# Kernel tuning notes

Measured on AMD Instinct MI355X. Metric: run time of the kernel, lower is better.

The kernel has to match this reference:

```python
import jax, jax.numpy as jnp
import numpy as np

H = 12          # trees_num / n_heads
D_WEIGHT = 0.1  # opt['d_weight']
NEG = -1e9


def setup_inputs() -> dict:
    key = jax.random.key(0)
    ks = jax.random.split(key, 6)
    B, N, D = 8, 512, 768
    inp = {}
    inp["input"] = jax.random.normal(ks[0], (B, N, D), dtype=jnp.float32)
    inp["src_mask"] = jax.random.randint(ks[1], (B, 1, N), 0, 2).astype(jnp.int32)
    inp["dep_emb"] = jax.random.normal(ks[2], (B, N, N), dtype=jnp.float32)
    s = 1.0 / np.sqrt(D)
    inp["Wq"] = jax.random.normal(ks[3], (D, D), dtype=jnp.float32) * s
    inp["bq"] = jnp.zeros((D,), dtype=jnp.float32)
    inp["Wk"] = jax.random.normal(ks[4], (D, D), dtype=jnp.float32) * s
    inp["bk"] = jnp.zeros((D,), dtype=jnp.float32)
    return inp


def reference(input, src_mask, dep_emb, Wq, bq, Wk, bk):
    B, N, D = input.shape
    dk = D // H
    # Q/K projections -> [B, H, N, dk]
    q = (input @ Wq + bq).reshape(B, N, H, dk).transpose(0, 2, 1, 3)
    k = (input @ Wk + bk).reshape(B, N, H, dk).transpose(0, 2, 1, 3)
    # scaled scores [B, H, N, N]
    scores = jnp.einsum("bhqd,bhkd->bhqk", q, k) / jnp.sqrt(jnp.asarray(dk, input.dtype))
    # blend with dependency bias: dep_emb [B,N,N] -> [B,1,N,N]
    scores = (1.0 - D_WEIGHT) * scores + D_WEIGHT * dep_emb[:, None, :, :]
    # mask: src_mask [B,1,N] -> [B,1,1,N]; masked_fill(mask==0, -1e9)
    scores = jnp.where(src_mask[:, None, :, :] == 0, NEG, scores)
    p_attn = jax.nn.softmax(scores, axis=-1)  # [B, H, N, N]
    # original returns list of per-head [B,N,N]; full tensor is equivalent
    return p_attn
```

## Files before the change

### kernel.cpp

```cpp
#include <hip/hip_runtime.h>


typedef _Float16 f16;
typedef _Float16 f16x4 __attribute__((ext_vector_type(4)));
typedef _Float16 f16x8 __attribute__((ext_vector_type(8)));
typedef float    f32x4 __attribute__((ext_vector_type(4)));

#define NTOK   512
#define DMODEL 768
#define BATCH  8
#define NHEAD  12
#define NEGV   (-1e9f)
#define DEPS   516

#define GLOAD_LDS16(g, l)                                                        \
    __builtin_amdgcn_global_load_lds(                                            \
        (const __attribute__((address_space(1))) void*)(g),                      \
        (__attribute__((address_space(3))) void*)(l), 16, 0, 0)

__global__ __launch_bounds__(256)
void prep_kernel(const float* __restrict__ X, f16* __restrict__ Xh,
                 const float* __restrict__ Wq, const float* __restrict__ Wk,
                 f16* __restrict__ Wt) {
    const int bx = blockIdx.x;
    if (bx < 3072) {
        const size_t i = ((size_t)bx * 256 + threadIdx.x) * 4;
        float4 v = *(const float4*)&X[i];
        f16x4 h = { (f16)v.x, (f16)v.y, (f16)v.z, (f16)v.w };
        *(f16x4*)&Xh[i] = h;
    } else {
        __shared__ float tile[32][33];
        const int id = bx - 3072;
        const int kb = (id % 24) * 32;
        const int nb = (id / 24) * 32;
        const float* __restrict__ W = (nb < 768) ? Wq : Wk;
        const int nc = (nb < 768) ? nb : nb - 768;
        const int tx = threadIdx.x & 31, ty = threadIdx.x >> 5;
        #pragma unroll
        for (int i = 0; i < 4; ++i)
            tile[ty + i*8][tx] = W[(size_t)(kb + ty + i*8) * DMODEL + nc + tx];
        __syncthreads();
        #pragma unroll
        for (int i = 0; i < 4; ++i)
            Wt[(size_t)(nb + ty + i*8) * DMODEL + kb + tx] = (f16)tile[tx][ty + i*8];
    }
}

__global__ __launch_bounds__(256)
void proj_mfma(const f16* __restrict__ Xh, const f16* __restrict__ Wt,
               const float* __restrict__ bq, const float* __restrict__ bk,
               f16* __restrict__ QK) {
    const int m0 = blockIdx.x * 128;
    const int n0 = blockIdx.y * 128;
    const int tid = threadIdx.x;
    const int wid = tid >> 6, l = tid & 63;
    const int l15 = l & 15, quad = l >> 4;
    const int wm = (wid & 1) * 64;
    const int wn = (wid >> 1) * 64;

    __shared__ f16 As[128 * 64];
    __shared__ f16 Bs[128 * 64];

    f32x4 acc[4][4];
    #pragma unroll
    for (int i = 0; i < 4; ++i)
        #pragma unroll
        for (int j = 0; j < 4; ++j) acc[i][j] = (f32x4){0.f, 0.f, 0.f, 0.f};

    const int crow = l >> 3;
    const int ccol = (l & 7) * 8;

    for (int kt = 0; kt < DMODEL; kt += 64) {
        #pragma unroll
        for (int i = 0; i < 4; ++i) {
            const int c   = wid * 4 + i;
            const int row = c * 8 + crow;
            GLOAD_LDS16(Xh + (size_t)(m0 + row) * DMODEL + kt + ccol, &As[c * 512]);
            GLOAD_LDS16(Wt + (size_t)(n0 + row) * DMODEL + kt + ccol, &Bs[c * 512]);
        }
        __syncthreads();
        #pragma unroll
        for (int ks = 0; ks < 2; ++ks) {
            f16x8 a[4], b[4];
            #pragma unroll
            for (int mi = 0; mi < 4; ++mi)
                a[mi] = *(f16x8*)&As[(wm + mi*16 + l15) * 64 + ks*32 + quad*8];
            #pragma unroll
            for (int ni = 0; ni < 4; ++ni)
                b[ni] = *(f16x8*)&Bs[(wn + ni*16 + l15) * 64 + ks*32 + quad*8];
            #pragma unroll
            for (int mi = 0; mi < 4; ++mi)
                #pragma unroll
                for (int ni = 0; ni < 4; ++ni)
                    acc[mi][ni] = __builtin_amdgcn_mfma_f32_16x16x32_f16(
                        a[mi], b[ni], acc[mi][ni], 0, 0, 0);
        }
        __syncthreads();
    }

    const float SC = (1.0f - 0.1f) / 8.0f;
    #pragma unroll
    for (int ni = 0; ni < 4; ++ni) {
        const int col = n0 + wn + ni * 16 + l15;
        const bool isQ = (col < 768);
        const float bv = isQ ? bq[col] : bk[col - 768];
        const float sc = isQ ? SC : 1.0f;
        #pragma unroll
        for (int mi = 0; mi < 4; ++mi)
            #pragma unroll
            for (int r = 0; r < 4; ++r) {
                const int row = m0 + wm + mi * 16 + quad * 4 + r;
                QK[(size_t)row * 1536 + col] = (f16)((acc[mi][ni][r] + bv) * sc);
            }
    }
}

__global__ __launch_bounds__(384, 2)
void attn_mfma(const f16* __restrict__ QK, const float* __restrict__ dep,
               const int* __restrict__ mask, float* __restrict__ out) {
    const int qt = blockIdx.x;
    const int hg = blockIdx.y;
    const int b  = blockIdx.z;
    const int tid = threadIdx.x;
    const int wid = tid >> 6;
    const int l   = tid & 63;
    const int l15 = l & 15, quad = l >> 4;
    const int h  = hg * 6 + wid;
    const int q0 = qt * 16;

    __shared__ float depL[16 * DEPS];

    {
        const float* __restrict__ src = dep + ((size_t)b * NTOK + q0) * NTOK;
        #pragma unroll
        for (int i = 0; i < 6; ++i) {
            const int idx = tid + i * 384;
            if (idx < 2048) {
                const int row = idx >> 7, c4 = idx & 127;
                float4 v = *(const float4*)&src[(size_t)row * NTOK + c4 * 4];
                *(float4*)&depL[row * DEPS + c4 * 4] = v;
            }
        }
    }

    f32x4 acc[32];
    #pragma unroll
    for (int t = 0; t < 32; ++t) acc[t] = (f32x4){0.f, 0.f, 0.f, 0.f};

    const f16* __restrict__ Qb = QK + (size_t)(b * NTOK + q0 + l15) * 1536 + h * 64 + quad * 8;
    const f16x8 qf0 = *(const f16x8*)(Qb);
    const f16x8 qf1 = *(const f16x8*)(Qb + 32);

    const f16* __restrict__ Kb = QK + (size_t)(b * NTOK + l15) * 1536 + 768 + h * 64 + quad * 8;
    #pragma unroll
    for (int t = 0; t < 32; ++t) {
        f16x8 k0 = *(const f16x8*)(Kb + (size_t)(t * 16) * 1536);
        acc[t] = __builtin_amdgcn_mfma_f32_16x16x32_f16(k0, qf0, acc[t], 0, 0, 0);
        f16x8 k1 = *(const f16x8*)(Kb + (size_t)(t * 16) * 1536 + 32);
        acc[t] = __builtin_amdgcn_mfma_f32_16x16x32_f16(k1, qf1, acc[t], 0, 0, 0);
    }

    __syncthreads();

    const float DW = 0.1f;
    const int* __restrict__ mrow = mask + b * NTOK;
    float m = NEGV;
    #pragma unroll
    for (int t = 0; t < 32; ++t) {
        const int kc = t * 16 + quad * 4;
        const f32x4 dv = *(const f32x4*)&depL[l15 * DEPS + kc];
        const int4  mv = *(const int4*)&mrow[kc];
        const float s0 = acc[t][0] + DW * dv[0];
        const float s1 = acc[t][1] + DW * dv[1];
        const float s2 = acc[t][2] + DW * dv[2];
        const float s3 = acc[t][3] + DW * dv[3];
        acc[t][0] = mv.x ? s0 : NEGV;
        acc[t][1] = mv.y ? s1 : NEGV;
        acc[t][2] = mv.z ? s2 : NEGV;
        acc[t][3] = mv.w ? s3 : NEGV;
        m = fmaxf(m, fmaxf(fmaxf(acc[t][0], acc[t][1]), fmaxf(acc[t][2], acc[t][3])));
    }
    m = fmaxf(m, __shfl_xor(m, 16));
    m = fmaxf(m, __shfl_xor(m, 32));

    float sum = 0.f;
    #pragma unroll
    for (int t = 0; t < 32; ++t) {
        #pragma unroll
        for (int r = 0; r < 4; ++r) {
            const float e = __expf(acc[t][r] - m);
            acc[t][r] = e;
            sum += e;
        }
    }
    sum += __shfl_xor(sum, 16);
    sum += __shfl_xor(sum, 32);
    const float inv = 1.0f / sum;

    const size_t obase = ((size_t)((b * NHEAD + h) * NTOK) + q0 + l15) * NTOK + quad * 4;
    #pragma unroll
    for (int t = 0; t < 32; ++t) {
        f32x4 v = acc[t] * inv;
        *(f32x4*)&out[obase + (size_t)t * 16] = v;
    }
}

extern "C" void kernel_launch(void* const* d_in, const int* in_sizes, int n_in,
                              void* d_out, int out_size, void* d_ws, size_t ws_size,
                              hipStream_t stream) {
    const float* X    = (const float*)d_in[0];
    const int*   mask = (const int*)  d_in[1];
    const float* dep  = (const float*)d_in[2];
    const float* Wq   = (const float*)d_in[3];
    const float* bq   = (const float*)d_in[4];
    const float* Wk   = (const float*)d_in[5];
    const float* bk   = (const float*)d_in[6];
    float* out = (float*)d_out;

    f16* Xh = (f16*)d_ws;
    f16* Wt = Xh + (size_t)BATCH * NTOK * DMODEL;
    f16* QK = Wt + (size_t)1536 * DMODEL;

    prep_kernel<<<dim3(3072 + 1152), 256, 0, stream>>>(X, Xh, Wq, Wk, Wt);
    proj_mfma<<<dim3(4096 / 128, 1536 / 128), 256, 0, stream>>>(Xh, Wt, bq, bk, QK);
    attn_mfma<<<dim3(32, 2, BATCH), 384, 0, stream>>>(QK, dep, mask, out);
}
```

Before: 190.7 us.

## Fuse Q projection into attention kernel, project only K separately

```diff
diff --git a/kernel.cpp b/kernel.cpp
--- a/kernel.cpp
+++ b/kernel.cpp
@@ -5,6 +5,7 @@
 typedef _Float16 f16x4 __attribute__((ext_vector_type(4)));
 typedef _Float16 f16x8 __attribute__((ext_vector_type(8)));
 typedef float    f32x4 __attribute__((ext_vector_type(4)));
+typedef unsigned int u32;
 
 #define NTOK   512
 #define DMODEL 768
@@ -47,9 +48,8 @@
 }
 
 __global__ __launch_bounds__(256)
-void proj_mfma(const f16* __restrict__ Xh, const f16* __restrict__ Wt,
-               const float* __restrict__ bq, const float* __restrict__ bk,
-               f16* __restrict__ QK) {
+void projk_mfma(const f16* __restrict__ Xh, const f16* __restrict__ Wt,
+                const float* __restrict__ bk, f16* __restrict__ Kh) {
     const int m0 = blockIdx.x * 128;
     const int n0 = blockIdx.y * 128;
     const int tid = threadIdx.x;
@@ -76,7 +76,7 @@
             const int c   = wid * 4 + i;
             const int row = c * 8 + crow;
             GLOAD_LDS16(Xh + (size_t)(m0 + row) * DMODEL + kt + ccol, &As[c * 512]);
-            GLOAD_LDS16(Wt + (size_t)(n0 + row) * DMODEL + kt + ccol, &Bs[c * 512]);
+            GLOAD_LDS16(Wt + (size_t)(768 + n0 + row) * DMODEL + kt + ccol, &Bs[c * 512]);
         }
         __syncthreads();
         #pragma unroll
@@ -98,26 +98,25 @@
         __syncthreads();
     }
 
-    const float SC = (1.0f - 0.1f) / 8.0f;
     #pragma unroll
     for (int ni = 0; ni < 4; ++ni) {
         const int col = n0 + wn + ni * 16 + l15;
-        const bool isQ = (col < 768);
-        const float bv = isQ ? bq[col] : bk[col - 768];
-        const float sc = isQ ? SC : 1.0f;
+        const float bv = bk[col];
         #pragma unroll
         for (int mi = 0; mi < 4; ++mi)
             #pragma unroll
             for (int r = 0; r < 4; ++r) {
                 const int row = m0 + wm + mi * 16 + quad * 4 + r;
-                QK[(size_t)row * 1536 + col] = (f16)((acc[mi][ni][r] + bv) * sc);
+                Kh[(size_t)row * DMODEL + col] = (f16)(acc[mi][ni][r] + bv);
             }
     }
 }
 
 __global__ __launch_bounds__(384, 2)
-void attn_mfma(const f16* __restrict__ QK, const float* __restrict__ dep,
-               const int* __restrict__ mask, float* __restrict__ out) {
+void attn_mfma(const f16* __restrict__ Xh, const f16* __restrict__ Wt,
+               const float* __restrict__ bq, const f16* __restrict__ Kh,
+               const float* __restrict__ dep, const int* __restrict__ mask,
+               float* __restrict__ out) {
     const int qt = blockIdx.x;
     const int hg = blockIdx.y;
     const int b  = blockIdx.z;
@@ -143,20 +142,66 @@
         }
     }
 
+    f32x4 accq[4];
+    #pragma unroll
+    for (int t = 0; t < 4; ++t) accq[t] = (f32x4){0.f, 0.f, 0.f, 0.f};
+    {
+        const f16* __restrict__ xb = Xh + ((size_t)(b * NTOK + q0 + l15)) * DMODEL + quad * 8;
+        const f16* __restrict__ wb = Wt + ((size_t)(h * 64 + l15)) * DMODEL + quad * 8;
+        #pragma unroll 4
+        for (int kt = 0; kt < 24; ++kt) {
+            const f16x8 xf = *(const f16x8*)(xb + kt * 32);
+            #pragma unroll
+            for (int t16 = 0; t16 < 4; ++t16) {
+                const f16x8 af = *(const f16x8*)(wb + (size_t)(t16 * 16) * DMODEL + kt * 32);
+                accq[t16] = __builtin_amdgcn_mfma_f32_16x16x32_f16(af, xf, accq[t16], 0, 0, 0);
+            }
+        }
+    }
+
+    const float SC = (1.0f - 0.1f) / 8.0f;
+    uint2 qh[4];
+    #pragma unroll
+    for (int t16 = 0; t16 < 4; ++t16) {
+        const int dbase = h * 64 + t16 * 16 + quad * 4;
+        union { uint2 u; f16x4 hv; } p;
+        #pragma unroll
+        for (int r = 0; r < 4; ++r)
+            p.hv[r] = (f16)((accq[t16][r] + bq[dbase + r]) * SC);
+        qh[t16] = p.u;
+    }
+    const int srcA = l15 + ((quad & 1) << 5);
+    const int srcB = srcA + 16;
+    #define SH(v, s) ((u32)__shfl((int)(v), (s)))
+    const bool hi = (quad >> 1) != 0;
+    u32 a0x = SH(qh[0].x, srcA), a0y = SH(qh[0].y, srcA);
+    u32 a1x = SH(qh[1].x, srcA), a1y = SH(qh[1].y, srcA);
+    u32 b0x = SH(qh[0].x, srcB), b0y = SH(qh[0].y, srcB);
+    u32 b1x = SH(qh[1].x, srcB), b1y = SH(qh[1].y, srcB);
+    union { uint4 u; f16x8 hv; } u0;
+    u0.u.x = hi ? a1x : a0x;  u0.u.y = hi ? a1y : a0y;
+    u0.u.z = hi ? b1x : b0x;  u0.u.w = hi ? b1y : b0y;
+    const f16x8 qf0 = u0.hv;
+    u32 c2x = SH(qh[2].x, srcA), c2y = SH(qh[2].y, srcA);
+    u32 c3x = SH(qh[3].x, srcA), c3y = SH(qh[3].y, srcA);
+    u32 d2x = SH(qh[2].x, srcB), d2y = SH(qh[2].y, srcB);
+    u32 d3x = SH(qh[3].x, srcB), d3y = SH(qh[3].y, srcB);
+    union { uint4 u; f16x8 hv; } u1;
+    u1.u.x = hi ? c3x : c2x;  u1.u.y = hi ? c3y : c2y;
+    u1.u.z = hi ? d3x : d2x;  u1.u.w = hi ? d3y : d2y;
+    const f16x8 qf1 = u1.hv;
+    #undef SH
+
     f32x4 acc[32];
     #pragma unroll
     for (int t = 0; t < 32; ++t) acc[t] = (f32x4){0.f, 0.f, 0.f, 0.f};
 
-    const f16* __restrict__ Qb = QK + (size_t)(b * NTOK + q0 + l15) * 1536 + h * 64 + quad * 8;
-    const f16x8 qf0 = *(const f16x8*)(Qb);
-    const f16x8 qf1 = *(const f16x8*)(Qb + 32);
-
-    const f16* __restrict__ Kb = QK + (size_t)(b * NTOK + l15) * 1536 + 768 + h * 64 + quad * 8;
-    #pragma unroll
-    for (int t = 0; t < 32; ++t) {
-        f16x8 k0 = *(const f16x8*)(Kb + (size_t)(t * 16) * 1536);
+    const f16* __restrict__ Kb = Kh + (size_t)(b * NTOK + l15) * DMODEL + h * 64 + quad * 8;
+    #pragma unroll
+    for (int t = 0; t < 32; ++t) {
+        f16x8 k0 = *(const f16x8*)(Kb + (size_t)(t * 16) * DMODEL);
         acc[t] = __builtin_amdgcn_mfma_f32_16x16x32_f16(k0, qf0, acc[t], 0, 0, 0);
-        f16x8 k1 = *(const f16x8*)(Kb + (size_t)(t * 16) * 1536 + 32);
+        f16x8 k1 = *(const f16x8*)(Kb + (size_t)(t * 16) * DMODEL + 32);
         acc[t] = __builtin_amdgcn_mfma_f32_16x16x32_f16(k1, qf1, acc[t], 0, 0, 0);
     }
 
@@ -219,9 +264,9 @@
 
     f16* Xh = (f16*)d_ws;
     f16* Wt = Xh + (size_t)BATCH * NTOK * DMODEL;
-    f16* QK = Wt + (size_t)1536 * DMODEL;
+    f16* Kh = Wt + (size_t)1536 * DMODEL;
 
     prep_kernel<<<dim3(3072 + 1152), 256, 0, stream>>>(X, Xh, Wq, Wk, Wt);
-    proj_mfma<<<dim3(4096 / 128, 1536 / 128), 256, 0, stream>>>(Xh, Wt, bq, bk, QK);
-    attn_mfma<<<dim3(32, 2, BATCH), 384, 0, stream>>>(QK, dep, mask, out);
-}
+    projk_mfma<<<dim3(4096 / 128, 768 / 128), 256, 0, stream>>>(Xh, Wt, bk, Kh);
+    attn_mfma<<<dim3(32, 2, BATCH), 384, 0, stream>>>(Xh, Wt, bq, Kh, dep, mask, out);
+}
```

Result: slower. 222.5 us (+16.7%).
